# Performance work log

Hardware: AMD Instinct MI355X
Metric: run time of the kernel (lower is better)

The kernel has to match this reference:

```python
import jax, jax.numpy as jnp
import numpy as np

N = 100000
IN_DIM = 512
HID = 5
HEADS1 = 5
NUM_CLASSES = 3
NEG_SLOPE = 0.2


def _gat_conv(x, src, dst, W, a_src, a_dst, b, heads, out_ch, concat):
    """PyG-style GATConv (eval mode, self-loops already included in src/dst)."""
    n = x.shape[0]
    h = (x @ W).reshape(n, heads, out_ch)                      # [N,H,C]
    alpha_src = jnp.einsum('nhc,hc->nh', h, a_src)             # [N,H]
    alpha_dst = jnp.einsum('nhc,hc->nh', h, a_dst)             # [N,H]
    e = jax.nn.leaky_relu(alpha_src[src] + alpha_dst[dst], NEG_SLOPE)  # [E,H]
    # segment softmax over edges grouped by destination node
    m = jax.ops.segment_max(e, dst, num_segments=n)            # [N,H]
    ex = jnp.exp(e - m[dst])
    denom = jax.ops.segment_sum(ex, dst, num_segments=n)       # [N,H]
    alpha = ex / denom[dst]                                    # [E,H]
    out = jax.ops.segment_sum(alpha[:, :, None] * h[src], dst, num_segments=n)  # [N,H,C]
    out = out.reshape(n, heads * out_ch) if concat else out.mean(axis=1)
    return out + b


def setup_inputs() -> dict:
    key = jax.random.key(0)
    ks = jax.random.split(key, 10)
    E = 3200000
    x = jax.random.normal(ks[0], (N, IN_DIM), dtype=jnp.float32)
    edge_index = jax.random.randint(ks[1], (2, E), 0, N, dtype=jnp.int64)
    s1 = 1.0 / np.sqrt(IN_DIM)
    s2 = 1.0 / np.sqrt(HID * HEADS1)
    return {
        'x': x,
        'edge_index': edge_index,
        'W1': jax.random.normal(ks[2], (IN_DIM, HEADS1 * HID), dtype=jnp.float32) * s1,
        'att_src1': jax.random.normal(ks[3], (HEADS1, HID), dtype=jnp.float32),
        'att_dst1': jax.random.normal(ks[4], (HEADS1, HID), dtype=jnp.float32),
        'bias1': jnp.zeros((HEADS1 * HID,), dtype=jnp.float32),
        'W2': jax.random.normal(ks[5], (HEADS1 * HID, NUM_CLASSES), dtype=jnp.float32) * s2,
        'att_src2': jax.random.normal(ks[6], (1, NUM_CLASSES), dtype=jnp.float32),
        'att_dst2': jax.random.normal(ks[7], (1, NUM_CLASSES), dtype=jnp.float32),
        'bias2': jnp.zeros((NUM_CLASSES,), dtype=jnp.float32),
    }


def reference(x, edge_index, W1, att_src1, att_dst1, bias1, W2, att_src2, att_dst2, bias2):
    # add self loops (PyG GATConv default)
    loops = jnp.arange(N, dtype=edge_index.dtype)
    src = jnp.concatenate([edge_index[0], loops])
    dst = jnp.concatenate([edge_index[1], loops])
    h = _gat_conv(x, src, dst, W1, att_src1, att_dst1, bias1, HEADS1, HID, True)
    h = jax.nn.elu(h)
    out = _gat_conv(h, src, dst, W2, att_src2, att_dst2, bias2, 1, NUM_CLASSES, False)
    return jax.nn.log_sigmoid(out)
```

## Files before the change

kernel.cpp:

```cpp
#include <hip/hip_runtime.h>
#include <math.h>

#define N_NODES 100000
#define IN_DIM  512
#define HID     5
#define HEADS   5
#define C1      25
#define NC      3
#define NEG     0.2f
#define NPB     64
#define BSH     7
#define NBUCK   ((N_NODES + 127) >> BSH)
#define NDIG    1024
#define NBH2    512
#define HTH2    256
#define BCAP    6144

typedef float f32x4 __attribute__((ext_vector_type(4)));

struct __attribute__((packed, aligned(4))) H6 { _Float16 a; _Float16 h[5]; };

__device__ __forceinline__ float lrelu(float v) { return v >= 0.f ? v : NEG * v; }

__device__ __forceinline__ void fma4(float acc[C1], f32x4 xv, const float* w) {
#pragma unroll
    for (int j = 0; j < C1; ++j)
        acc[j] = __builtin_fmaf(xv.w, w[3 * C1 + j],
                 __builtin_fmaf(xv.z, w[2 * C1 + j],
                 __builtin_fmaf(xv.y, w[C1 + j],
                 __builtin_fmaf(xv.x, w[j], acc[j]))));
}

__global__ void __launch_bounds__(256)
k_gemm_hist(const float* __restrict__ x, const float* __restrict__ W1,
            const float* __restrict__ as1, const float* __restrict__ ad1,
            const int* __restrict__ ei, int E, int TOT, int NG,
            _Float16* __restrict__ h1p, float* __restrict__ adst,
            int* __restrict__ hist) {
    __shared__ float red[3][64][C1];
    int b = blockIdx.x;
    int tid = threadIdx.x;
    if (b >= NG) {
        int* lh = (int*)red;
        int hb = b - NG;
        for (int i = tid; i < NDIG; i += HTH2) lh[i] = 0;
        __syncthreads();
        int chunk = (TOT + NBH2 - 1) / NBH2;
        int e0 = hb * chunk, e1 = min(e0 + chunk, TOT);
        for (int e = e0 + tid; e < e1; e += HTH2) {
            int d = (e < E) ? ei[E + e] : e - E;
            atomicAdd(&lh[d >> BSH], 1);
        }
        __syncthreads();
        for (int i = tid; i < NDIG; i += HTH2) hist[hb * NDIG + i] = lh[i];
        return;
    }
    int c = __builtin_amdgcn_readfirstlane(tid >> 6);
    int l = tid & 63;
    int n = b * 64 + l;
    int nc = n < N_NODES ? n : N_NODES - 1;
    const f32x4* xr = (const f32x4*)(x + (size_t)nc * IN_DIM) + c * 32;
    const float* Wb = W1 + (size_t)c * 128 * C1;
    float acc[C1];
#pragma unroll
    for (int j = 0; j < C1; ++j) acc[j] = 0.f;
    for (int L = 0; L < 8; ++L) {
        f32x4 xv[4];
#pragma unroll
        for (int q = 0; q < 4; ++q) xv[q] = xr[L * 4 + q];
#pragma unroll
        for (int q = 0; q < 4; ++q)
            fma4(acc, xv[q], Wb + (size_t)(L * 4 + q) * 4 * C1);
    }
    if (c > 0) {
#pragma unroll
        for (int j = 0; j < C1; ++j) red[c - 1][l][j] = acc[j];
    }
    __syncthreads();
    if (c == 0 && n < N_NODES) {
#pragma unroll
        for (int j = 0; j < C1; ++j)
            acc[j] += red[0][l][j] + red[1][l][j] + red[2][l][j];
        _Float16 hb16[32];
#pragma unroll
        for (int h = 0; h < HEADS; ++h) {
            float s = 0.f, d = 0.f;
#pragma unroll
            for (int cc = 0; cc < HID; ++cc) {
                s += acc[h * HID + cc] * as1[h * HID + cc];
                d += acc[h * HID + cc] * ad1[h * HID + cc];
                hb16[6 * h + 1 + cc] = (_Float16)acc[h * HID + cc];
            }
            hb16[6 * h] = (_Float16)s;
            adst[n * HEADS + h] = d;
        }
        hb16[30] = (_Float16)0.f; hb16[31] = (_Float16)0.f;
        float4* h4 = (float4*)(h1p + (size_t)n * 32);
        const float4* src = (const float4*)hb16;
#pragma unroll
        for (int q = 0; q < 4; ++q) h4[q] = src[q];
    }
}

__global__ void __launch_bounds__(NBH2)
k_colscan(int* __restrict__ hist, int* __restrict__ bcnt) {
    __shared__ int sh[NBH2];
    int d = blockIdx.x, t = threadIdx.x;
    int v = hist[t * NDIG + d];
    sh[t] = v;
    __syncthreads();
    for (int ofs = 1; ofs < NBH2; ofs <<= 1) {
        int u = (t >= ofs) ? sh[t - ofs] : 0;
        __syncthreads();
        sh[t] += u;
        __syncthreads();
    }
    hist[t * NDIG + d] = sh[t] - v;
    if (t == NBH2 - 1) bcnt[d] = sh[t];
}

__global__ void __launch_bounds__(NDIG)
k_boff(const int* __restrict__ bcnt, int* __restrict__ boff) {
    __shared__ int sh[NDIG];
    int t = threadIdx.x;
    int v = bcnt[t];
    sh[t] = v;
    __syncthreads();
    for (int ofs = 1; ofs < NDIG; ofs <<= 1) {
        int u = (t >= ofs) ? sh[t - ofs] : 0;
        __syncthreads();
        sh[t] += u;
        __syncthreads();
    }
    boff[t] = sh[t] - v;
}

__global__ void __launch_bounds__(HTH2)
k_write(const int* __restrict__ ei, int E, int TOT, const int* __restrict__ hist,
        const int* __restrict__ boff, int* __restrict__ pk) {
    __shared__ int lbase[NDIG];
    __shared__ int lcur[NDIG];
    int b = blockIdx.x, tid = threadIdx.x;
    for (int i = tid; i < NDIG; i += HTH2) {
        lbase[i] = boff[i] + hist[b * NDIG + i];
        lcur[i] = 0;
    }
    __syncthreads();
    int chunk = (TOT + NBH2 - 1) / NBH2;
    int e0 = b * chunk, e1 = min(e0 + chunk, TOT);
    for (int e = e0 + tid; e < e1; e += HTH2) {
        int s, d;
        if (e < E) { s = ei[e]; d = ei[E + e]; } else { s = d = e - E; }
        int dg = d >> BSH;
        int r = atomicAdd(&lcur[dg], 1);
        pk[lbase[dg] + r] = s | ((d & 127) << 17);
    }
}

__global__ void __launch_bounds__(512)
k_bgroup(const int* __restrict__ boff, const int* __restrict__ bcnt,
         const int* __restrict__ pk, int* __restrict__ off, int* __restrict__ deg,
         int* __restrict__ ssrc) {
    __shared__ int stage[BCAP];
    __shared__ int cnt[128], pref[128], lcur[128];
    int b = blockIdx.x, tid = threadIdx.x;
    int n0 = b << BSH;
    if (tid < 128) cnt[tid] = 0;
    __syncthreads();
    int r0 = boff[b], total = bcnt[b];
    for (int idx = tid; idx < total; idx += 512) {
        int v = pk[r0 + idx];
        if (idx < BCAP) stage[idx] = v;
        atomicAdd(&cnt[(v >> 17) & 127], 1);
    }
    __syncthreads();
    if (tid < 128) pref[tid] = cnt[tid];
    __syncthreads();
    for (int ofs = 1; ofs < 128; ofs <<= 1) {
        int u = 0;
        if (tid < 128 && tid >= ofs) u = pref[tid - ofs];
        __syncthreads();
        if (tid < 128) pref[tid] += u;
        __syncthreads();
    }
    if (tid < 128) {
        int n = n0 + tid;
        if (n < N_NODES) {
            off[n] = r0 + pref[tid] - cnt[tid];
            deg[n] = cnt[tid];
        }
        lcur[tid] = 0;
    }
    __syncthreads();
    for (int idx = tid; idx < total; idx += 512) {
        int v = (idx < BCAP) ? stage[idx] : pk[r0 + idx];
        int dl = (v >> 17) & 127;
        int r = atomicAdd(&lcur[dl], 1);
        ssrc[r0 + pref[dl] - cnt[dl] + r] = v & 0x1FFFF;
    }
}

__global__ void __launch_bounds__(NPB * HEADS)
k_layer1(const int* __restrict__ off, const int* __restrict__ deg, const int* __restrict__ ssrc,
         const _Float16* __restrict__ h1p, const float* __restrict__ adst,
         const float* __restrict__ b1, const float* __restrict__ W2,
         const float* __restrict__ as2, const float* __restrict__ ad2,
         float4* __restrict__ n2, float* __restrict__ a2d) {
    __shared__ float sh[NPB * C1];
    int tid = threadIdx.x;
    int ln = tid / HEADS, h = tid % HEADS;
    int n = blockIdx.x * NPB + ln;
    if (n < N_NODES) {
        int st = off[n], cnt = deg[n];
        float adn = adst[n * HEADS + h];
        float den = 0.f;
        float num[HID] = {0.f, 0.f, 0.f, 0.f, 0.f};
        const _Float16* hp = (const _Float16*)h1p + 6 * h;
        int i = 0;
        for (; i + 1 < cnt; i += 2) {
            int s0 = ssrc[st + i];
            int s1 = ssrc[st + i + 1];
            H6 hv0 = *(const H6*)(hp + (size_t)s0 * 32);
            H6 hv1 = *(const H6*)(hp + (size_t)s1 * 32);
            float p0 = __expf(lrelu((float)hv0.a + adn));
            float p1 = __expf(lrelu((float)hv1.a + adn));
            den += p0 + p1;
#pragma unroll
            for (int c = 0; c < HID; ++c) {
                num[c] = __builtin_fmaf(p0, (float)hv0.h[c], num[c]);
                num[c] = __builtin_fmaf(p1, (float)hv1.h[c], num[c]);
            }
        }
        if (i < cnt) {
            int s = ssrc[st + i];
            H6 hv = *(const H6*)(hp + (size_t)s * 32);
            float p = __expf(lrelu((float)hv.a + adn));
            den += p;
#pragma unroll
            for (int c = 0; c < HID; ++c) num[c] = __builtin_fmaf(p, (float)hv.h[c], num[c]);
        }
        float inv = 1.f / den;
#pragma unroll
        for (int c = 0; c < HID; ++c) {
            float v = num[c] * inv + b1[h * HID + c];
            sh[ln * C1 + h * HID + c] = v > 0.f ? v : expm1f(v);
        }
    }
    __syncthreads();
    if (tid < NPB) {
        int nn = blockIdx.x * NPB + tid;
        if (nn < N_NODES) {
            float gg[NC] = {0.f, 0.f, 0.f};
#pragma unroll
            for (int j = 0; j < C1; ++j) {
                float hv = sh[tid * C1 + j];
#pragma unroll
                for (int c = 0; c < NC; ++c) gg[c] += hv * W2[j * NC + c];
            }
            float ssv = 0.f, ddv = 0.f;
#pragma unroll
            for (int c = 0; c < NC; ++c) { ssv += gg[c] * as2[c]; ddv += gg[c] * ad2[c]; }
            n2[nn] = make_float4(ssv, gg[0], gg[1], gg[2]);
            a2d[nn] = ddv;
        }
    }
}

__global__ void k_layer2(const int* __restrict__ off, const int* __restrict__ deg,
                         const int* __restrict__ ssrc, const float4* __restrict__ n2,
                         const float* __restrict__ a2d, const float* __restrict__ b2,
                         float* __restrict__ out) {
    int n = blockIdx.x * blockDim.x + threadIdx.x;
    if (n >= N_NODES) return;
    int st = off[n], cnt = deg[n];
    float adn = a2d[n];
    float den = 0.f, num0 = 0.f, num1 = 0.f, num2 = 0.f;
    int i = 0;
    for (; i + 1 < cnt; i += 2) {
        int s0 = ssrc[st + i];
        int s1 = ssrc[st + i + 1];
        float4 g0 = n2[s0];
        float4 g1 = n2[s1];
        float p0 = __expf(lrelu(g0.x + adn));
        float p1 = __expf(lrelu(g1.x + adn));
        den += p0 + p1;
        num0 = __builtin_fmaf(p0, g0.y, __builtin_fmaf(p1, g1.y, num0));
        num1 = __builtin_fmaf(p0, g0.z, __builtin_fmaf(p1, g1.z, num1));
        num2 = __builtin_fmaf(p0, g0.w, __builtin_fmaf(p1, g1.w, num2));
    }
    if (i < cnt) {
        int s = ssrc[st + i];
        float4 gv = n2[s];
        float p = __expf(lrelu(gv.x + adn));
        den += p;
        num0 = __builtin_fmaf(p, gv.y, num0);
        num1 = __builtin_fmaf(p, gv.z, num1);
        num2 = __builtin_fmaf(p, gv.w, num2);
    }
    float inv = 1.f / den;
    float vv[NC] = {num0 * inv + b2[0], num1 * inv + b2[1], num2 * inv + b2[2]};
#pragma unroll
    for (int c = 0; c < NC; ++c) {
        float v = vv[c];
        out[n * NC + c] = (v >= 0.f) ? -log1pf(__expf(-v)) : v - log1pf(__expf(v));
    }
}

extern "C" void kernel_launch(void* const* d_in, const int* in_sizes, int n_in,
                              void* d_out, int out_size, void* d_ws, size_t ws_size,
                              hipStream_t stream) {
    const float* x   = (const float*)d_in[0];
    const int*   ei  = (const int*)d_in[1];
    const float* W1  = (const float*)d_in[2];
    const float* as1 = (const float*)d_in[3];
    const float* ad1 = (const float*)d_in[4];
    const float* b1  = (const float*)d_in[5];
    const float* W2  = (const float*)d_in[6];
    const float* as2 = (const float*)d_in[7];
    const float* ad2 = (const float*)d_in[8];
    const float* b2  = (const float*)d_in[9];
    float* out = (float*)d_out;
    int E = in_sizes[1] / 2;
    int TOT = E + N_NODES;

    int*   iws = (int*)d_ws;
    float* fws = (float*)d_ws;
    int* hist = iws;
    int* bcnt = iws + 524288;
    int* boff = iws + 525312;
    int* off  = iws + 526336;
    int* deg  = iws + 626336;
    int* pk   = iws + 726336;
    int* ssrc = pk + TOT;
    size_t fbase = 726336 + 2 * (size_t)TOT;
    _Float16* h1p = (_Float16*)(fws + fbase);
    float*  adst = fws + fbase + 1600000;
    float4* n2   = (float4*)(fws + fbase + 2100000);
    float*  a2d  = fws + fbase + 2500000;

    dim3 blk(256);
    int NB1 = (N_NODES + 255) / 256;
    int NG  = (N_NODES + 63) / 64;
    k_gemm_hist<<<dim3(NG + NBH2), dim3(256), 0, stream>>>(
        x, W1, as1, ad1, ei, E, TOT, NG, h1p, adst, hist);
    k_colscan<<<dim3(NDIG), dim3(NBH2), 0, stream>>>(hist, bcnt);
    k_boff<<<dim3(1), dim3(NDIG), 0, stream>>>(bcnt, boff);
    k_write<<<dim3(NBH2), dim3(HTH2), 0, stream>>>(ei, E, TOT, hist, boff, pk);
    k_bgroup<<<dim3(NBUCK), dim3(512), 0, stream>>>(boff, bcnt, pk, off, deg, ssrc);
    k_layer1<<<dim3((N_NODES + NPB - 1) / NPB), dim3(NPB * HEADS), 0, stream>>>(
        off, deg, ssrc, h1p, adst, b1, W2, as2, ad2, n2, a2d);
    k_layer2<<<dim3(NB1), blk, 0, stream>>>(off, deg, ssrc, n2, a2d, b2, out);
}
```

Before: 262.9 us.

## Fold bucket-offset scan into consumers and unroll gather loops by four

Removes the single-block k_boff launch. k_write now recomputes the exclusive scan over bucket counts itself, and k_bgroup computes its own start offset with a block reduction over preceding counts. This saves one kernel launch and one dependency, at the cost of redundant scan work in every block. The edge-gather loops in both GAT layers are also unrolled to four edges per iteration to expose more independent loads in flight.

```diff
diff --git a/kernel.cpp b/kernel.cpp
--- a/kernel.cpp
+++ b/kernel.cpp
@@ -119,55 +119,61 @@
     if (t == NBH2 - 1) bcnt[d] = sh[t];
 }
 
-__global__ void __launch_bounds__(NDIG)
-k_boff(const int* __restrict__ bcnt, int* __restrict__ boff) {
-    __shared__ int sh[NDIG];
-    int t = threadIdx.x;
-    int v = bcnt[t];
-    sh[t] = v;
-    __syncthreads();
-    for (int ofs = 1; ofs < NDIG; ofs <<= 1) {
-        int u = (t >= ofs) ? sh[t - ofs] : 0;
-        __syncthreads();
-        sh[t] += u;
-        __syncthreads();
-    }
-    boff[t] = sh[t] - v;
-}
-
 __global__ void __launch_bounds__(HTH2)
 k_write(const int* __restrict__ ei, int E, int TOT, const int* __restrict__ hist,
-        const int* __restrict__ boff, int* __restrict__ pk) {
+        const int* __restrict__ bcnt, int* __restrict__ pk) {
     __shared__ int lbase[NDIG];
     __shared__ int lcur[NDIG];
-    int b = blockIdx.x, tid = threadIdx.x;
-    for (int i = tid; i < NDIG; i += HTH2) {
-        lbase[i] = boff[i] + hist[b * NDIG + i];
-        lcur[i] = 0;
-    }
+    __shared__ int ssum[HTH2];
+    int b = blockIdx.x, t = threadIdx.x;
+    int q0 = bcnt[4 * t], q1 = bcnt[4 * t + 1], q2 = bcnt[4 * t + 2], q3 = bcnt[4 * t + 3];
+    int s = q0 + q1 + q2 + q3;
+    ssum[t] = s;
+    __syncthreads();
+    for (int ofs = 1; ofs < HTH2; ofs <<= 1) {
+        int u = (t >= ofs) ? ssum[t - ofs] : 0;
+        __syncthreads();
+        ssum[t] += u;
+        __syncthreads();
+    }
+    int base = ssum[t] - s;
+    const int* hb = hist + (size_t)b * NDIG;
+    lbase[4 * t]     = base + hb[4 * t];
+    lbase[4 * t + 1] = base + q0 + hb[4 * t + 1];
+    lbase[4 * t + 2] = base + q0 + q1 + hb[4 * t + 2];
+    lbase[4 * t + 3] = base + q0 + q1 + q2 + hb[4 * t + 3];
+    lcur[4 * t] = 0; lcur[4 * t + 1] = 0; lcur[4 * t + 2] = 0; lcur[4 * t + 3] = 0;
     __syncthreads();
     int chunk = (TOT + NBH2 - 1) / NBH2;
     int e0 = b * chunk, e1 = min(e0 + chunk, TOT);
-    for (int e = e0 + tid; e < e1; e += HTH2) {
-        int s, d;
-        if (e < E) { s = ei[e]; d = ei[E + e]; } else { s = d = e - E; }
+    for (int e = e0 + t; e < e1; e += HTH2) {
+        int src, d;
+        if (e < E) { src = ei[e]; d = ei[E + e]; } else { src = d = e - E; }
         int dg = d >> BSH;
         int r = atomicAdd(&lcur[dg], 1);
-        pk[lbase[dg] + r] = s | ((d & 127) << 17);
+        pk[lbase[dg] + r] = src | ((d & 127) << 17);
     }
 }
 
 __global__ void __launch_bounds__(512)
-k_bgroup(const int* __restrict__ boff, const int* __restrict__ bcnt,
-         const int* __restrict__ pk, int* __restrict__ off, int* __restrict__ deg,
-         int* __restrict__ ssrc) {
+k_bgroup(const int* __restrict__ bcnt, const int* __restrict__ pk,
+         int* __restrict__ off, int* __restrict__ deg, int* __restrict__ ssrc) {
     __shared__ int stage[BCAP];
+    __shared__ int rsum[512];
     __shared__ int cnt[128], pref[128], lcur[128];
     int b = blockIdx.x, tid = threadIdx.x;
     int n0 = b << BSH;
+    int part = 0;
+    for (int i = tid; i < b; i += 512) part += bcnt[i];
+    rsum[tid] = part;
     if (tid < 128) cnt[tid] = 0;
     __syncthreads();
-    int r0 = boff[b], total = bcnt[b];
+    for (int ofs = 256; ofs > 0; ofs >>= 1) {
+        if (tid < ofs) rsum[tid] += rsum[tid + ofs];
+        __syncthreads();
+    }
+    int r0 = rsum[0];
+    int total = bcnt[b];
     for (int idx = tid; idx < total; idx += 512) {
         int v = pk[r0 + idx];
         if (idx < BCAP) stage[idx] = v;
@@ -217,18 +223,40 @@
         float num[HID] = {0.f, 0.f, 0.f, 0.f, 0.f};
         const _Float16* hp = (const _Float16*)h1p + 6 * h;
         int i = 0;
+        for (; i + 3 < cnt; i += 4) {
+            int s0 = ssrc[st + i];
+            int s1 = ssrc[st + i + 1];
+            int s2 = ssrc[st + i + 2];
+            int s3 = ssrc[st + i + 3];
+            H6 v0 = *(const H6*)(hp + (size_t)s0 * 32);
+            H6 v1 = *(const H6*)(hp + (size_t)s1 * 32);
+            H6 v2 = *(const H6*)(hp + (size_t)s2 * 32);
+            H6 v3 = *(const H6*)(hp + (size_t)s3 * 32);
+            float p0 = __expf(lrelu((float)v0.a + adn));
+            float p1 = __expf(lrelu((float)v1.a + adn));
+            float p2 = __expf(lrelu((float)v2.a + adn));
+            float p3 = __expf(lrelu((float)v3.a + adn));
+            den += (p0 + p1) + (p2 + p3);
+#pragma unroll
+            for (int c = 0; c < HID; ++c) {
+                num[c] = __builtin_fmaf(p0, (float)v0.h[c], num[c]);
+                num[c] = __builtin_fmaf(p1, (float)v1.h[c], num[c]);
+                num[c] = __builtin_fmaf(p2, (float)v2.h[c], num[c]);
+                num[c] = __builtin_fmaf(p3, (float)v3.h[c], num[c]);
+            }
+        }
         for (; i + 1 < cnt; i += 2) {
             int s0 = ssrc[st + i];
             int s1 = ssrc[st + i + 1];
-            H6 hv0 = *(const H6*)(hp + (size_t)s0 * 32);
-            H6 hv1 = *(const H6*)(hp + (size_t)s1 * 32);
-            float p0 = __expf(lrelu((float)hv0.a + adn));
-            float p1 = __expf(lrelu((float)hv1.a + adn));
+            H6 v0 = *(const H6*)(hp + (size_t)s0 * 32);
+            H6 v1 = *(const H6*)(hp + (size_t)s1 * 32);
+            float p0 = __expf(lrelu((float)v0.a + adn));
+            float p1 = __expf(lrelu((float)v1.a + adn));
             den += p0 + p1;
 #pragma unroll
             for (int c = 0; c < HID; ++c) {
-                num[c] = __builtin_fmaf(p0, (float)hv0.h[c], num[c]);
-                num[c] = __builtin_fmaf(p1, (float)hv1.h[c], num[c]);
+                num[c] = __builtin_fmaf(p0, (float)v0.h[c], num[c]);
+                num[c] = __builtin_fmaf(p1, (float)v1.h[c], num[c]);
             }
         }
         if (i < cnt) {
@@ -276,19 +304,28 @@
     float adn = a2d[n];
     float den = 0.f, num0 = 0.f, num1 = 0.f, num2 = 0.f;
     int i = 0;
-    for (; i + 1 < cnt; i += 2) {
+    for (; i + 3 < cnt; i += 4) {
         int s0 = ssrc[st + i];
         int s1 = ssrc[st + i + 1];
+        int s2 = ssrc[st + i + 2];
+        int s3 = ssrc[st + i + 3];
         float4 g0 = n2[s0];
         float4 g1 = n2[s1];
+        float4 g2 = n2[s2];
+        float4 g3 = n2[s3];
         float p0 = __expf(lrelu(g0.x + adn));
         float p1 = __expf(lrelu(g1.x + adn));
-        den += p0 + p1;
-        num0 = __builtin_fmaf(p0, g0.y, __builtin_fmaf(p1, g1.y, num0));
-        num1 = __builtin_fmaf(p0, g0.z, __builtin_fmaf(p1, g1.z, num1));
-        num2 = __builtin_fmaf(p0, g0.w, __builtin_fmaf(p1, g1.w, num2));
-    }
-    if (i < cnt) {
+        float p2 = __expf(lrelu(g2.x + adn));
+        float p3 = __expf(lrelu(g3.x + adn));
+        den += (p0 + p1) + (p2 + p3);
+        num0 = __builtin_fmaf(p0, g0.y, __builtin_fmaf(p1, g1.y,
+               __builtin_fmaf(p2, g2.y, __builtin_fmaf(p3, g3.y, num0))));
+        num1 = __builtin_fmaf(p0, g0.z, __builtin_fmaf(p1, g1.z,
+               __builtin_fmaf(p2, g2.z, __builtin_fmaf(p3, g3.z, num1))));
+        num2 = __builtin_fmaf(p0, g0.w, __builtin_fmaf(p1, g1.w,
+               __builtin_fmaf(p2, g2.w, __builtin_fmaf(p3, g3.w, num2))));
+    }
+    for (; i < cnt; ++i) {
         int s = ssrc[st + i];
         float4 gv = n2[s];
         float p = __expf(lrelu(gv.x + adn));
@@ -327,7 +364,6 @@
     float* fws = (float*)d_ws;
     int* hist = iws;
     int* bcnt = iws + 524288;
-    int* boff = iws + 525312;
     int* off  = iws + 526336;
     int* deg  = iws + 626336;
     int* pk   = iws + 726336;
@@ -344,9 +380,8 @@
     k_gemm_hist<<<dim3(NG + NBH2), dim3(256), 0, stream>>>(
         x, W1, as1, ad1, ei, E, TOT, NG, h1p, adst, hist);
     k_colscan<<<dim3(NDIG), dim3(NBH2), 0, stream>>>(hist, bcnt);
-    k_boff<<<dim3(1), dim3(NDIG), 0, stream>>>(bcnt, boff);
-    k_write<<<dim3(NBH2), dim3(HTH2), 0, stream>>>(ei, E, TOT, hist, boff, pk);
-    k_bgroup<<<dim3(NBUCK), dim3(512), 0, stream>>>(boff, bcnt, pk, off, deg, ssrc);
+    k_write<<<dim3(NBH2), dim3(HTH2), 0, stream>>>(ei, E, TOT, hist, bcnt, pk);
+    k_bgroup<<<dim3(NBUCK), dim3(512), 0, stream>>>(bcnt, pk, off, deg, ssrc);
     k_layer1<<<dim3((N_NODES + NPB - 1) / NPB), dim3(NPB * HEADS), 0, stream>>>(
         off, deg, ssrc, h1p, adst, b1, W2, as2, ad2, n2, a2d);
     k_layer2<<<dim3(NB1), blk, 0, stream>>>(off, deg, ssrc, n2, a2d, b2, out);
```

New measurement: 242.2 us. 7.9% less time.
